# Performance work log

Hardware: AMD Instinct MI355X
Metric: run time of the kernel (lower is better)

## Reference

```python
import jax, jax.numpy as jnp
import numpy as np
from jax import lax

TAG_SIZE = 512
START_TAG = 510  # tag2idx['START_TAG']
STOP_TAG = 511   # tag2idx['STOP_TAG']
NEG_INF = -10000.0


def setup_inputs() -> dict:
    key = jax.random.key(0)
    k1, k2, k3 = jax.random.split(key, 3)
    B, T, K = 64, 1024, TAG_SIZE
    feats = jax.random.normal(k1, (B, T, K), dtype=jnp.float32)
    transitions = jax.random.normal(k2, (K, K), dtype=jnp.float32)
    # lengths in [1, T] (length 0 would make the original's backtrace ill-defined)
    lengths = jax.random.randint(k3, (B,), 1, T + 1, dtype=jnp.int64)
    return {"feats": feats, "transitions": transitions, "lengths": lengths}


def _viterbi_one(feats, length, transitions):
    """Viterbi decode one sequence. feats: [T, K]. Returns (score, path [T]).

    Padded steps (t >= length) leave the viterbi state unchanged and emit -1
    in the returned path (original returns a python list of len==length).
    """
    T, K = feats.shape
    init_fv = jnp.full((K,), NEG_INF, dtype=feats.dtype).at[START_TAG].set(0.0)

    def step(fv, inp):
        t, feat = inp
        # scores[next, prev] = fv[prev] + transitions[next, prev]
        scores = fv[None, :] + transitions
        bptr = jnp.argmax(scores, axis=1)              # [K] best prev per next tag
        vit = jnp.max(scores, axis=1) + feat           # [K]
        new_fv = jnp.where(t < length, vit, fv)
        return new_fv, bptr

    fv, bptrs = lax.scan(step, init_fv, (jnp.arange(T), feats))
    terminal = fv + transitions[STOP_TAG]
    best = jnp.argmax(terminal)
    score = terminal[best]

    def back(tag, inp):
        t, bp = inp
        valid = t < length
        emit = jnp.where(valid, tag, -1)
        new_tag = jnp.where(valid, bp[tag], tag)
        return new_tag, emit

    _, path_rev = lax.scan(back, best, (jnp.arange(T)[::-1], bptrs[::-1]))
    path = path_rev[::-1]
    return score, path


def reference(feats, transitions, lengths):
    # Original loops over the batch decoding each sequence but only the last
    # iteration's (score, tag_seq) survives; we decode all sequences
    # vectorized with vmap (same per-sequence work) and return the last.
    scores, paths = jax.vmap(_viterbi_one, in_axes=(0, 0, None))(
        feats, lengths, transitions
    )
    return scores[-1], paths[-1]
```

## Files before the change

### kernel.cpp

```cpp
#include <hip/hip_runtime.h>
#include <stdint.h>


#define KK 512
#define TMAX 1024
#define STARTT 510
#define STOPT 511
#define NEGINF (-10000.0f)
#define DSLOT 8

#define WS_FV 0
#define WS_BEST 32768
#define WS_BP 40960
#define WS_E (40960 + 1048576)

__device__ __forceinline__ int read_len(const void* lp) {
  const int* q = (const int*)lp;
  return (q[1] == 0) ? (int)(((const long long*)lp)[63]) : q[63];
}

__global__ void k_init(char* ws) {
  uint64_t* fvb = (uint64_t*)(ws + WS_FV);
  int tid = threadIdx.x;
  float v = (tid == STARTT) ? 0.0f : NEGINF;
  fvb[tid] = (uint64_t)__float_as_uint(v);
#pragma unroll
  for (int b = 1; b < DSLOT; ++b) fvb[b * KK + tid] = 0x7FFFFFFF00000000ull;
}

__global__ void __launch_bounds__(64) k_forward(
    const float* __restrict__ feats, const float* __restrict__ trans,
    const void* __restrict__ lens, float* __restrict__ out, char* ws) {
  const int len = read_len(lens);
  const int w = blockIdx.x;
  const int l = threadIdx.x;
  const int c = l & 31;
  const int R = 2 * w + (l >> 5);
  uint64_t* fvb = (uint64_t*)(ws + WS_FV);
  uint16_t* bp = (uint16_t*)(ws + WS_BP);

  float tr[16];
#pragma unroll
  for (int k = 0; k < 16; ++k) tr[k] = trans[(size_t)R * KK + c + 32 * k];

  const float* fb = feats + 63ll * TMAX * KK;
  const bool leader = (c == 0);
  float featNext = leader ? fb[R] : 0.0f;

  for (int t = 0; t < len; ++t) {
    uint64_t* slot = fvb + (size_t)(t & (DSLOT - 1)) * KK;
    uint64_t v[8];
    bool ok;
    do {
#pragma unroll
      for (int m = 0; m < 8; ++m)
        v[m] = __hip_atomic_load(&slot[l + 64 * m], __ATOMIC_RELAXED, __HIP_MEMORY_SCOPE_AGENT);
      ok = true;
#pragma unroll
      for (int m = 0; m < 8; ++m) ok = ok && ((int)(uint32_t)(v[m] >> 32) == t);
    } while (__any(!ok));
    float fvals[8];
#pragma unroll
    for (int m = 0; m < 8; ++m) fvals[m] = __uint_as_float((uint32_t)v[m]);

    const float featCur = featNext;
    if (leader && t + 1 < len) featNext = fb[(size_t)(t + 1) * KK + R];

    float bv;
    int bj;
#pragma unroll
    for (int k = 0; k < 16; ++k) {
      float fvk = __shfl(fvals[k >> 1], c + 32 * (k & 1));
      float cand = fvk + tr[k];
      if (k == 0) {
        bv = cand; bj = c;
      } else if (cand > bv) {
        bv = cand; bj = c + 32 * k;
      }
    }
#pragma unroll
    for (int m = 16; m >= 1; m >>= 1) {
      float ov = __shfl_xor(bv, m);
      int oj = __shfl_xor(bj, m);
      if (ov > bv || (ov == bv && oj < bj)) { bv = ov; bj = oj; }
    }
    if (leader) {
      const float vit = bv + featCur;
      const uint64_t pk = ((uint64_t)(uint32_t)(t + 1) << 32) | (uint64_t)__float_as_uint(vit);
      __hip_atomic_store(&fvb[(size_t)((t + 1) & (DSLOT - 1)) * KK + R], pk,
                         __ATOMIC_RELAXED, __HIP_MEMORY_SCOPE_AGENT);
      bp[(size_t)t * KK + R] = (uint16_t)bj;
    }
  }

  if (w != 0) return;
  {
    uint64_t* slot = fvb + (size_t)(len & (DSLOT - 1)) * KK;
    uint64_t v[8];
    bool ok;
    do {
#pragma unroll
      for (int m = 0; m < 8; ++m)
        v[m] = __hip_atomic_load(&slot[l + 64 * m], __ATOMIC_RELAXED, __HIP_MEMORY_SCOPE_AGENT);
      ok = true;
#pragma unroll
      for (int m = 0; m < 8; ++m) ok = ok && ((int)(uint32_t)(v[m] >> 32) == len);
    } while (__any(!ok));
    float tv;
    int tj;
#pragma unroll
    for (int m = 0; m < 8; ++m) {
      float x = __uint_as_float((uint32_t)v[m]) + trans[(size_t)STOPT * KK + l + 64 * m];
      if (m == 0) {
        tv = x; tj = l;
      } else if (x > tv) {
        tv = x; tj = l + 64 * m;
      }
    }
#pragma unroll
    for (int m = 32; m >= 1; m >>= 1) {
      float ov = __shfl_xor(tv, m);
      int oj = __shfl_xor(tj, m);
      if (ov > tv || (ov == tv && oj < tj)) { tv = ov; tj = oj; }
    }
    if (l == 0) {
      out[0] = tv;
      *((int*)(ws + WS_BEST)) = tj;
    }
  }
}

__global__ void __launch_bounds__(512) k_walk(const void* __restrict__ lens, char* ws) {
  const int len = read_len(lens);
  const uint16_t* bp = (const uint16_t*)(ws + WS_BP);
  uint16_t* E = (uint16_t*)(ws + WS_E);
  const int s = blockIdx.x;
  const int k = threadIdx.x;
  int tag = k;
  const int lo = s * 16;
  for (int t = lo + 15; t >= lo; --t)
    if (t < len) tag = bp[(size_t)t * KK + tag];
  E[s * KK + k] = (uint16_t)tag;
}

__global__ void __launch_bounds__(64) k_emit(
    const void* __restrict__ lens, float* __restrict__ out, char* ws) {
  const int len = read_len(lens);
  const uint16_t* bp = (const uint16_t*)(ws + WS_BP);
  const uint16_t* E = (const uint16_t*)(ws + WS_E);
  __shared__ int entry[64];
  const int tid = threadIdx.x;
  if (tid == 0) {
    int st = *((const int*)(ws + WS_BEST));
    for (int s = 63; s >= 0; --s) { entry[s] = st; st = E[s * KK + st]; }
  }
  __syncthreads();
  {
    const int s = tid;
    int st = entry[s];
    for (int t = s * 16 + 15; t >= s * 16; --t) {
      if (t < len) {
        out[1 + t] = (float)st;
        st = bp[(size_t)t * KK + st];
      } else {
        out[1 + t] = -1.0f;
      }
    }
  }
}

extern "C" void kernel_launch(void* const* d_in, const int* in_sizes, int n_in,
                              void* d_out, int out_size, void* d_ws, size_t ws_size,
                              hipStream_t stream) {
  const float* feats = (const float*)d_in[0];
  const float* trans = (const float*)d_in[1];
  const void* lens = d_in[2];
  float* out = (float*)d_out;
  char* ws = (char*)d_ws;
  (void)in_sizes; (void)n_in; (void)out_size; (void)ws_size;

  k_init<<<1, 512, 0, stream>>>(ws);
  k_forward<<<256, 64, 0, stream>>>(feats, trans, lens, out, ws);
  k_walk<<<64, 512, 0, stream>>>(lens, ws);
  k_emit<<<1, 64, 0, stream>>>(lens, out, ws);
}
```

Baseline: 646.4 us.

## Assign one forward row per wave and replace shuffles with local argmax tree

Each forward block now owns a single next-tag row across a full 64-lane wave instead of two rows per wave split into 32-lane halves. Each lane reduces its eight prev-tag candidates locally with a tie-aware pairwise tree, so the per-step __shfl broadcasts of fv values are gone. A 6-level xor reduction then finishes the argmax. The change doubles the number of blocks that poll the shared fv slots every step, which adds global memory polling traffic and synchronisation pressure in exchange for a shorter per-step critical path.

```diff
diff --git a/kernel.cpp b/kernel.cpp
--- a/kernel.cpp
+++ b/kernel.cpp
@@ -32,20 +32,17 @@
     const float* __restrict__ feats, const float* __restrict__ trans,
     const void* __restrict__ lens, float* __restrict__ out, char* ws) {
   const int len = read_len(lens);
-  const int w = blockIdx.x;
+  const int R = blockIdx.x;
   const int l = threadIdx.x;
-  const int c = l & 31;
-  const int R = 2 * w + (l >> 5);
   uint64_t* fvb = (uint64_t*)(ws + WS_FV);
   uint16_t* bp = (uint16_t*)(ws + WS_BP);
 
-  float tr[16];
+  float tr[8];
 #pragma unroll
-  for (int k = 0; k < 16; ++k) tr[k] = trans[(size_t)R * KK + c + 32 * k];
+  for (int m = 0; m < 8; ++m) tr[m] = trans[(size_t)R * KK + l + 64 * m];
 
   const float* fb = feats + 63ll * TMAX * KK;
-  const bool leader = (c == 0);
-  float featNext = leader ? fb[R] : 0.0f;
+  float featNext = fb[R];
 
   for (int t = 0; t < len; ++t) {
     uint64_t* slot = fvb + (size_t)(t & (DSLOT - 1)) * KK;
@@ -59,32 +56,37 @@
 #pragma unroll
       for (int m = 0; m < 8; ++m) ok = ok && ((int)(uint32_t)(v[m] >> 32) == t);
     } while (__any(!ok));
-    float fvals[8];
-#pragma unroll
-    for (int m = 0; m < 8; ++m) fvals[m] = __uint_as_float((uint32_t)v[m]);
 
     const float featCur = featNext;
-    if (leader && t + 1 < len) featNext = fb[(size_t)(t + 1) * KK + R];
+    if (t + 1 < len) featNext = fb[(size_t)(t + 1) * KK + R];
 
-    float bv;
-    int bj;
+    float c0[8];
 #pragma unroll
-    for (int k = 0; k < 16; ++k) {
-      float fvk = __shfl(fvals[k >> 1], c + 32 * (k & 1));
-      float cand = fvk + tr[k];
-      if (k == 0) {
-        bv = cand; bj = c;
-      } else if (cand > bv) {
-        bv = cand; bj = c + 32 * k;
-      }
+    for (int m = 0; m < 8; ++m) c0[m] = __uint_as_float((uint32_t)v[m]) + tr[m];
+    float v4[4]; int i4[4];
+#pragma unroll
+    for (int m = 0; m < 4; ++m) {
+      const bool L = c0[2 * m] >= c0[2 * m + 1];
+      v4[m] = L ? c0[2 * m] : c0[2 * m + 1];
+      i4[m] = L ? 2 * m : 2 * m + 1;
     }
+    float v2[2]; int i2[2];
 #pragma unroll
-    for (int m = 16; m >= 1; m >>= 1) {
+    for (int m = 0; m < 2; ++m) {
+      const bool L = v4[2 * m] >= v4[2 * m + 1];
+      v2[m] = L ? v4[2 * m] : v4[2 * m + 1];
+      i2[m] = L ? i4[2 * m] : i4[2 * m + 1];
+    }
+    const bool L = v2[0] >= v2[1];
+    float bv = L ? v2[0] : v2[1];
+    int bj = l + 64 * (L ? i2[0] : i2[1]);
+#pragma unroll
+    for (int m = 32; m >= 1; m >>= 1) {
       float ov = __shfl_xor(bv, m);
       int oj = __shfl_xor(bj, m);
       if (ov > bv || (ov == bv && oj < bj)) { bv = ov; bj = oj; }
     }
-    if (leader) {
+    if (l == 0) {
       const float vit = bv + featCur;
       const uint64_t pk = ((uint64_t)(uint32_t)(t + 1) << 32) | (uint64_t)__float_as_uint(vit);
       __hip_atomic_store(&fvb[(size_t)((t + 1) & (DSLOT - 1)) * KK + R], pk,
@@ -93,7 +95,7 @@
     }
   }
 
-  if (w != 0) return;
+  if (R != 0) return;
   {
     uint64_t* slot = fvb + (size_t)(len & (DSLOT - 1)) * KK;
     uint64_t v[8];
@@ -180,7 +182,7 @@
   (void)in_sizes; (void)n_in; (void)out_size; (void)ws_size;
 
   k_init<<<1, 512, 0, stream>>>(ws);
-  k_forward<<<256, 64, 0, stream>>>(feats, trans, lens, out, ws);
+  k_forward<<<512, 64, 0, stream>>>(feats, trans, lens, out, ws);
   k_walk<<<64, 512, 0, stream>>>(lens, ws);
   k_emit<<<1, 64, 0, stream>>>(lens, out, ws);
 }
```

Result: slower. 1.513 ms (+134.0%).

## Replicate forward-state broadcast buffer to spread polling traffic across copies

Applied to the files above, without the earlier changes.

The shared Viterbi state ring buffer, which all 256 blocks poll each timestep, is replicated up to 8 times. Each block polls its own replica, and each producer writes its result to every replica. The aim is to reduce contention on the same cache lines from many spinning readers, at the cost of more atomic stores per step from each leader. The copy count is chosen from the available workspace size, and the workspace layout is reordered so the state buffers sit at the end.

```diff
diff --git a/kernel.cpp b/kernel.cpp
--- a/kernel.cpp
+++ b/kernel.cpp
@@ -9,34 +9,38 @@
 #define NEGINF (-10000.0f)
 #define DSLOT 8
 
-#define WS_FV 0
-#define WS_BEST 32768
-#define WS_BP 40960
-#define WS_E (40960 + 1048576)
+#define WS_BP 0
+#define WS_E 1048576
+#define WS_BEST 1114112
+#define WS_FV 1114176
 
 __device__ __forceinline__ int read_len(const void* lp) {
   const int* q = (const int*)lp;
   return (q[1] == 0) ? (int)(((const long long*)lp)[63]) : q[63];
 }
 
-__global__ void k_init(char* ws) {
+__global__ void k_init(char* ws, int ncopy) {
   uint64_t* fvb = (uint64_t*)(ws + WS_FV);
-  int tid = threadIdx.x;
-  float v = (tid == STARTT) ? 0.0f : NEGINF;
-  fvb[tid] = (uint64_t)__float_as_uint(v);
-#pragma unroll
-  for (int b = 1; b < DSLOT; ++b) fvb[b * KK + tid] = 0x7FFFFFFF00000000ull;
+  const int tid = threadIdx.x;
+  const float v0 = (tid == STARTT) ? 0.0f : NEGINF;
+  const uint64_t iv = (uint64_t)__float_as_uint(v0);
+  for (int rp = 0; rp < ncopy; ++rp) {
+    uint64_t* rep = fvb + (size_t)rp * (DSLOT * KK);
+    rep[tid] = iv;
+    for (int b = 1; b < DSLOT; ++b) rep[b * KK + tid] = 0x7FFFFFFF00000000ull;
+  }
 }
 
 __global__ void __launch_bounds__(64) k_forward(
     const float* __restrict__ feats, const float* __restrict__ trans,
-    const void* __restrict__ lens, float* __restrict__ out, char* ws) {
+    const void* __restrict__ lens, float* __restrict__ out, char* ws, int ncopy) {
   const int len = read_len(lens);
   const int w = blockIdx.x;
   const int l = threadIdx.x;
   const int c = l & 31;
   const int R = 2 * w + (l >> 5);
   uint64_t* fvb = (uint64_t*)(ws + WS_FV);
+  uint64_t* myrep = fvb + (size_t)(w & (ncopy - 1)) * (DSLOT * KK);
   uint16_t* bp = (uint16_t*)(ws + WS_BP);
 
   float tr[16];
@@ -48,7 +52,7 @@
   float featNext = leader ? fb[R] : 0.0f;
 
   for (int t = 0; t < len; ++t) {
-    uint64_t* slot = fvb + (size_t)(t & (DSLOT - 1)) * KK;
+    uint64_t* slot = myrep + (size_t)(t & (DSLOT - 1)) * KK;
     uint64_t v[8];
     bool ok;
     do {
@@ -87,15 +91,17 @@
     if (leader) {
       const float vit = bv + featCur;
       const uint64_t pk = ((uint64_t)(uint32_t)(t + 1) << 32) | (uint64_t)__float_as_uint(vit);
-      __hip_atomic_store(&fvb[(size_t)((t + 1) & (DSLOT - 1)) * KK + R], pk,
-                         __ATOMIC_RELAXED, __HIP_MEMORY_SCOPE_AGENT);
+      const size_t so = (size_t)((t + 1) & (DSLOT - 1)) * KK + R;
+      for (int rp = 0; rp < ncopy; ++rp)
+        __hip_atomic_store(&fvb[(size_t)rp * (DSLOT * KK) + so], pk,
+                           __ATOMIC_RELAXED, __HIP_MEMORY_SCOPE_AGENT);
       bp[(size_t)t * KK + R] = (uint16_t)bj;
     }
   }
 
   if (w != 0) return;
   {
-    uint64_t* slot = fvb + (size_t)(len & (DSLOT - 1)) * KK;
+    uint64_t* slot = myrep + (size_t)(len & (DSLOT - 1)) * KK;
     uint64_t v[8];
     bool ok;
     do {
@@ -177,10 +183,16 @@
   const void* lens = d_in[2];
   float* out = (float*)d_out;
   char* ws = (char*)d_ws;
-  (void)in_sizes; (void)n_in; (void)out_size; (void)ws_size;
+  (void)in_sizes; (void)n_in; (void)out_size;
 
-  k_init<<<1, 512, 0, stream>>>(ws);
-  k_forward<<<256, 64, 0, stream>>>(feats, trans, lens, out, ws);
+  const size_t base = (size_t)WS_FV;
+  int ncopy = 1;
+  if (ws_size >= base + 8 * 32768) ncopy = 8;
+  else if (ws_size >= base + 4 * 32768) ncopy = 4;
+  else if (ws_size >= base + 2 * 32768) ncopy = 2;
+
+  k_init<<<1, 512, 0, stream>>>(ws, ncopy);
+  k_forward<<<256, 64, 0, stream>>>(feats, trans, lens, out, ws, ncopy);
   k_walk<<<64, 512, 0, stream>>>(lens, ws);
   k_emit<<<1, 64, 0, stream>>>(lens, out, ws);
 }
```

After: 660.0 us. +2.1%, slower.

## Merge fv values incrementally as they arrive in double-buffered polling loop

Applied to the files above, without the earlier changes.

The forward Viterbi step now polls the shared fv slot with two alternating load batches and folds each entry into the running max as soon as its tag matches, instead of spinning until all 512 entries are ready and only then computing. Each lane now covers both output rows across 64 columns, with a single 64-wide shuffle reduction in place of the per-half-wave layout and cross-lane fv broadcast shuffles. The workspace layout is reordered and launch bounds are set to one block per CU. This aims to overlap the max computation with waiting on other workgroups. It adds more branching and tie-breaking comparisons per element.

```diff
diff --git a/kernel.cpp b/kernel.cpp
--- a/kernel.cpp
+++ b/kernel.cpp
@@ -9,10 +9,10 @@
 #define NEGINF (-10000.0f)
 #define DSLOT 8
 
-#define WS_FV 0
-#define WS_BEST 32768
-#define WS_BP 40960
-#define WS_E (40960 + 1048576)
+#define WS_BP 0
+#define WS_E 1048576
+#define WS_BEST 1114112
+#define WS_FV 1114176
 
 __device__ __forceinline__ int read_len(const void* lp) {
   const int* q = (const int*)lp;
@@ -21,75 +21,88 @@
 
 __global__ void k_init(char* ws) {
   uint64_t* fvb = (uint64_t*)(ws + WS_FV);
-  int tid = threadIdx.x;
-  float v = (tid == STARTT) ? 0.0f : NEGINF;
-  fvb[tid] = (uint64_t)__float_as_uint(v);
+  const int tid = threadIdx.x;
+  const float v0 = (tid == STARTT) ? 0.0f : NEGINF;
+  fvb[tid] = (uint64_t)__float_as_uint(v0);
 #pragma unroll
   for (int b = 1; b < DSLOT; ++b) fvb[b * KK + tid] = 0x7FFFFFFF00000000ull;
 }
 
-__global__ void __launch_bounds__(64) k_forward(
+#define MERGE_BATCH(arr)                                                       \
+  _Pragma("unroll") for (int m = 0; m < 8; ++m) {                              \
+    if ((stale & (1u << m)) && (int)(uint32_t)(arr[m] >> 32) == t) {           \
+      stale &= ~(1u << m);                                                     \
+      const float val = __uint_as_float((uint32_t)arr[m]);                     \
+      const int j = l + 64 * m;                                                \
+      const float c0 = val + tr0[m];                                           \
+      if (c0 > bv0 || (c0 == bv0 && j < bj0)) { bv0 = c0; bj0 = j; }           \
+      const float c1 = val + tr1[m];                                           \
+      if (c1 > bv1 || (c1 == bv1 && j < bj1)) { bv1 = c1; bj1 = j; }           \
+    }                                                                          \
+  }
+
+__global__ void __launch_bounds__(64, 1) k_forward(
     const float* __restrict__ feats, const float* __restrict__ trans,
     const void* __restrict__ lens, float* __restrict__ out, char* ws) {
   const int len = read_len(lens);
   const int w = blockIdx.x;
   const int l = threadIdx.x;
-  const int c = l & 31;
-  const int R = 2 * w + (l >> 5);
+  const int R0 = 2 * w;
   uint64_t* fvb = (uint64_t*)(ws + WS_FV);
   uint16_t* bp = (uint16_t*)(ws + WS_BP);
 
-  float tr[16];
+  float tr0[8], tr1[8];
 #pragma unroll
-  for (int k = 0; k < 16; ++k) tr[k] = trans[(size_t)R * KK + c + 32 * k];
+  for (int m = 0; m < 8; ++m) {
+    tr0[m] = trans[(size_t)R0 * KK + l + 64 * m];
+    tr1[m] = trans[(size_t)(R0 + 1) * KK + l + 64 * m];
+  }
 
   const float* fb = feats + 63ll * TMAX * KK;
-  const bool leader = (c == 0);
-  float featNext = leader ? fb[R] : 0.0f;
+  float featNext = (l < 2) ? fb[R0 + l] : 0.0f;
 
   for (int t = 0; t < len; ++t) {
     uint64_t* slot = fvb + (size_t)(t & (DSLOT - 1)) * KK;
-    uint64_t v[8];
-    bool ok;
-    do {
+    float bv0 = -3.0e38f, bv1 = -3.0e38f;
+    int bj0 = 0x7fffffff, bj1 = 0x7fffffff;
+    uint32_t stale = 0xFFu;
+    uint64_t a[8], b[8];
+#pragma unroll
+    for (int m = 0; m < 8; ++m)
+      a[m] = __hip_atomic_load(&slot[l + 64 * m], __ATOMIC_RELAXED, __HIP_MEMORY_SCOPE_AGENT);
+    while (true) {
 #pragma unroll
       for (int m = 0; m < 8; ++m)
-        v[m] = __hip_atomic_load(&slot[l + 64 * m], __ATOMIC_RELAXED, __HIP_MEMORY_SCOPE_AGENT);
-      ok = true;
+        b[m] = __hip_atomic_load(&slot[l + 64 * m], __ATOMIC_RELAXED, __HIP_MEMORY_SCOPE_AGENT);
+      MERGE_BATCH(a)
+      if (!__any(stale != 0)) break;
 #pragma unroll
-      for (int m = 0; m < 8; ++m) ok = ok && ((int)(uint32_t)(v[m] >> 32) == t);
-    } while (__any(!ok));
-    float fvals[8];
-#pragma unroll
-    for (int m = 0; m < 8; ++m) fvals[m] = __uint_as_float((uint32_t)v[m]);
+      for (int m = 0; m < 8; ++m)
+        a[m] = __hip_atomic_load(&slot[l + 64 * m], __ATOMIC_RELAXED, __HIP_MEMORY_SCOPE_AGENT);
+      MERGE_BATCH(b)
+      if (!__any(stale != 0)) break;
+    }
 
     const float featCur = featNext;
-    if (leader && t + 1 < len) featNext = fb[(size_t)(t + 1) * KK + R];
+    if (l < 2 && t + 1 < len) featNext = fb[(size_t)(t + 1) * KK + R0 + l];
 
-    float bv;
-    int bj;
 #pragma unroll
-    for (int k = 0; k < 16; ++k) {
-      float fvk = __shfl(fvals[k >> 1], c + 32 * (k & 1));
-      float cand = fvk + tr[k];
-      if (k == 0) {
-        bv = cand; bj = c;
-      } else if (cand > bv) {
-        bv = cand; bj = c + 32 * k;
-      }
+    for (int m = 32; m >= 1; m >>= 1) {
+      const float ov0 = __shfl_xor(bv0, m);
+      const int oj0 = __shfl_xor(bj0, m);
+      const float ov1 = __shfl_xor(bv1, m);
+      const int oj1 = __shfl_xor(bj1, m);
+      if (ov0 > bv0 || (ov0 == bv0 && oj0 < bj0)) { bv0 = ov0; bj0 = oj0; }
+      if (ov1 > bv1 || (ov1 == bv1 && oj1 < bj1)) { bv1 = ov1; bj1 = oj1; }
     }
-#pragma unroll
-    for (int m = 16; m >= 1; m >>= 1) {
-      float ov = __shfl_xor(bv, m);
-      int oj = __shfl_xor(bj, m);
-      if (ov > bv || (ov == bv && oj < bj)) { bv = ov; bj = oj; }
-    }
-    if (leader) {
+    if (l < 2) {
+      const float bv = l ? bv1 : bv0;
+      const int bj = l ? bj1 : bj0;
       const float vit = bv + featCur;
       const uint64_t pk = ((uint64_t)(uint32_t)(t + 1) << 32) | (uint64_t)__float_as_uint(vit);
-      __hip_atomic_store(&fvb[(size_t)((t + 1) & (DSLOT - 1)) * KK + R], pk,
+      __hip_atomic_store(&fvb[(size_t)((t + 1) & (DSLOT - 1)) * KK + R0 + l], pk,
                          __ATOMIC_RELAXED, __HIP_MEMORY_SCOPE_AGENT);
-      bp[(size_t)t * KK + R] = (uint16_t)bj;
+      bp[(size_t)t * KK + R0 + l] = (uint16_t)bj;
     }
   }
 
```

Result: slower. 1.631 ms (+152.4%).
